# Performance work log

Hardware: AMD Instinct MI355X
Metric: run time of the kernel (lower is better)

The kernel has to match this reference:

```python
import jax, jax.numpy as jnp
import numpy as np

B, C, H, W = 4, 256, 160, 160
N = 512
REID = 128
NUM_LAYERS = 2
BINS = 7          # adaptive_avg_pool2d target (7,7)
EPS_BN = 1e-5
EPS_NORM = 1e-12  # torch F.normalize eps


def setup_inputs() -> dict:
    key = jax.random.key(0)
    ks = jax.random.split(key, 8)
    x = jax.random.normal(ks[0], (B, C, H, W), jnp.float32)
    # valid normalized boxes: x1,y1 in [0,0.7], w,h in [0.1,0.3]
    xy1 = jax.random.uniform(ks[1], (B, N, 2), minval=0.0, maxval=0.7)
    wh = jax.random.uniform(ks[2], (B, N, 2), minval=0.1, maxval=0.3)
    bboxes = jnp.concatenate([xy1, jnp.minimum(xy1 + wh, 1.0)], axis=-1)
    # conv stack params (kaiming-ish init), BN in eval mode with running stats
    conv_w = jax.random.normal(ks[3], (NUM_LAYERS, C, C, 3, 3), jnp.float32) * np.sqrt(2.0 / (C * 9)).astype(np.float32)
    conv_b = jnp.zeros((NUM_LAYERS, C), jnp.float32)
    bn_gamma = jnp.ones((NUM_LAYERS, C), jnp.float32)
    bn_beta = jnp.zeros((NUM_LAYERS, C), jnp.float32)
    bn_mean = jnp.zeros((NUM_LAYERS, C), jnp.float32)
    bn_var = jnp.ones((NUM_LAYERS, C), jnp.float32)
    # reid_embedding MLP: Linear(C, C//2) -> ReLU -> Dropout(eval) -> Linear(C//2, REID)
    w1 = jax.random.normal(ks[4], (C // 2, C), jnp.float32) * 0.01
    b1 = jnp.zeros((C // 2,), jnp.float32)
    w2 = jax.random.normal(ks[5], (REID, C // 2), jnp.float32) * 0.01
    b2 = jnp.zeros((REID,), jnp.float32)
    return dict(x=x, bboxes=bboxes, conv_w=conv_w, conv_b=conv_b,
                bn_gamma=bn_gamma, bn_beta=bn_beta, bn_mean=bn_mean, bn_var=bn_var,
                w1=w1, b1=b1, w2=w2, b2=b2)


def _conv_bn_relu(x, w, b, gamma, beta, mean, var):
    y = jax.lax.conv_general_dilated(
        x, w, window_strides=(1, 1), padding=((1, 1), (1, 1)),
        dimension_numbers=('NCHW', 'OIHW', 'NCHW')) + b[None, :, None, None]
    scale = (gamma / jnp.sqrt(var + EPS_BN))[None, :, None, None]
    y = (y - mean[None, :, None, None]) * scale + beta[None, :, None, None]
    return jax.nn.relu(y)


def _roi_pool(S, box):
    # S: (C, H+1, W+1) integral image of the feature map; box: (4,) = x1,y1,x2,y2 in [0,1]
    x1 = jnp.clip(jnp.floor(box[0] * W).astype(jnp.int32), 0, W)
    y1 = jnp.clip(jnp.floor(box[1] * H).astype(jnp.int32), 0, H)
    x2 = jnp.clip(jnp.floor(box[2] * W).astype(jnp.int32), 0, W)
    y2 = jnp.clip(jnp.floor(box[3] * H).astype(jnp.int32), 0, H)
    valid = (x2 > x1) & (y2 > y1)
    hl = jnp.maximum(y2 - y1, 1)
    wl = jnp.maximum(x2 - x1, 1)
    i = jnp.arange(BINS)
    # PyTorch adaptive_avg_pool2d binning: [floor(i*L/B), ceil((i+1)*L/B))
    hs = y1 + (i * hl) // BINS
    he = y1 + ((i + 1) * hl + BINS - 1) // BINS
    ws = x1 + (i * wl) // BINS
    we = x1 + ((i + 1) * wl + BINS - 1) // BINS
    # bin sums via integral image -> (C, 7, 7)
    s = (S[:, he[:, None], we[None, :]] - S[:, hs[:, None], we[None, :]]
         - S[:, he[:, None], ws[None, :]] + S[:, hs[:, None], ws[None, :]])
    area = ((he - hs)[:, None] * (we - ws)[None, :]).astype(S.dtype)
    # adaptive 7x7 avg pool, then global avg pool over the 7x7 grid
    pooled = jnp.mean(s / area, axis=(1, 2))  # (C,)
    return pooled, valid


def reference(x, bboxes, conv_w, conv_b, bn_gamma, bn_beta, bn_mean, bn_var, w1, b1, w2, b2):
    f = x
    for l in range(NUM_LAYERS):
        f = _conv_bn_relu(f, conv_w[l], conv_b[l], bn_gamma[l], bn_beta[l], bn_mean[l], bn_var[l])
    # integral image, zero-padded: S[b,c,y,x] = sum of f[b,c,:y,:x] -> (B, C, H+1, W+1)
    S = jnp.pad(jnp.cumsum(jnp.cumsum(f, axis=2), axis=3), ((0, 0), (0, 0), (1, 0), (1, 0)))
    pooled, valid = jax.vmap(jax.vmap(_roi_pool, in_axes=(None, 0)), in_axes=(0, 0))(S, bboxes)
    # reid_embedding MLP (dropout is identity in eval)
    h = jax.nn.relu(jnp.einsum('bnc,hc->bnh', pooled, w1) + b1)
    feat = jnp.einsum('bnh,rh->bnr', h, w2) + b2
    feat = jnp.where(valid[..., None], feat, jnp.zeros((), feat.dtype))
    norm = jnp.maximum(jnp.linalg.norm(feat, axis=-1, keepdims=True), EPS_NORM)
    return feat / norm
```

## Files before the change

### kernel.cpp

```cpp
#include <hip/hip_runtime.h>
#include <hip/hip_bf16.h>

typedef __attribute__((ext_vector_type(8))) short s16x8;
typedef __attribute__((ext_vector_type(4))) float f32x4;


__device__ __forceinline__ void async_ld16(const void* g, void* l) {
  __builtin_amdgcn_global_load_lds(
      (const __attribute__((address_space(1))) void*)g,
      (__attribute__((address_space(3))) void*)l, 16, 0, 0);
}

__global__ __launch_bounds__(256) void nchw2nhwc(const float* __restrict__ x,
                                                 __hip_bfloat16* __restrict__ xpad) {
  __shared__ float tile[32][33];
  int blk = blockIdx.x;
  int xt = blk % 5;
  int ct = (blk / 5) & 7;
  int by = blk / 40;
  int b = by / 160, y = by - (by / 160) * 160;
  int tx = threadIdx.x, ty = threadIdx.y;
  const float* src = x + (((size_t)(b * 256 + ct * 32)) * 160 + y) * 160 + xt * 32 + tx;
#pragma unroll
  for (int k = 0; k < 4; k++) tile[ty * 4 + k][tx] = src[(size_t)(ty * 4 + k) * 25600];
  __syncthreads();
  __hip_bfloat16* dst = xpad + (((size_t)(b * 162 + y + 1)) * 162 + (xt * 32 + 1)) * 256 + ct * 32 + tx;
#pragma unroll
  for (int k = 0; k < 4; k++) {
    int xx = ty * 4 + k;
    dst[(size_t)xx * 256] = __float2bfloat16(tile[tx][xx]);
  }
}

__global__ __launch_bounds__(256) void pack_w(const float* __restrict__ cw,
                                              __hip_bfloat16* __restrict__ wpk) {
  int t = blockIdx.x * 256 + threadIdx.x;
  int ci = t & 255, co = (t >> 8) & 255, rest = t >> 16;
  int tap = rest % 9, l = rest / 9;
  int dy = tap / 3, dx = tap - dy * 3;
  float v = cw[((((size_t)l * 256 + co) * 256 + ci) * 3 + dy) * 3 + dx];
  wpk[(((size_t)l * 9 + tap) * 256 + co) * 256 + ci] = __float2bfloat16(v);
}

__global__ void prep_bn(const float* __restrict__ cb, const float* __restrict__ g,
                        const float* __restrict__ bt, const float* __restrict__ mn,
                        const float* __restrict__ vr, float* __restrict__ ab) {
  int t = blockIdx.x * 256 + threadIdx.x;
  float a = g[t] / sqrtf(vr[t] + 1e-5f);
  ab[t] = a;
  ab[512 + t] = (cb[t] - mn[t]) * a + bt[t];
}

__global__ __launch_bounds__(256) void conv_bn_relu(
    const __hip_bfloat16* __restrict__ inp, __hip_bfloat16* __restrict__ outp,
    const __hip_bfloat16* __restrict__ wpk,
    const float* __restrict__ alpha, const float* __restrict__ beff) {
  __shared__ __align__(16) short As[128 * 64];
  __shared__ __align__(16) short Bs[128 * 64];
  const int t = threadIdx.x;
  const int logical = ((blockIdx.x & 7) * 200) + (blockIdx.x >> 3);
  const int mtile = logical >> 1;
  const int ntile = logical & 1;
  const int l = t & 63, wv = t >> 6;
  const int lr = l & 15, lq = l >> 4;
  const int wm = wv >> 1, wn = wv & 1;
  const int co0 = ntile << 7;

  const int srow = t >> 3;
  const int koff = (((t & 7) ^ (srow & 7)) << 3);
  const short* inS = (const short*)inp;
  const short* wS = (const short*)wpk;
  long abase[4];
#pragma unroll
  for (int i = 0; i < 4; i++) {
    int p = mtile * 128 + i * 32 + srow;
    int b = p / 25600; int r = p - b * 25600; int y = r / 160; int x = r - y * 160;
    abase[i] = (((long)b * 162 + y) * 162 + x) * 256 + koff;
  }
  const long bbase = ((long)(co0 + srow)) * 256 + koff;
  short* aldst = As + t * 8;
  short* bldst = Bs + t * 8;

  f32x4 acc[4][4];
#pragma unroll
  for (int i = 0; i < 4; i++)
#pragma unroll
    for (int j = 0; j < 4; j++) acc[i][j] = (f32x4){0.f, 0.f, 0.f, 0.f};

#pragma unroll 1
  for (int tap = 0; tap < 9; ++tap) {
    const int dy = tap / 3, dx = tap - dy * 3;
    const long atap = ((long)dy * 162 + dx) * 256;
    const long btap = (long)tap * 65536;
#pragma unroll
    for (int kc = 0; kc < 4; ++kc) {
      const long ko = (long)kc * 64;
      __syncthreads();
#pragma unroll
      for (int i = 0; i < 4; i++)
        async_ld16(inS + abase[i] + atap + ko, aldst + i * 2048);
#pragma unroll
      for (int i = 0; i < 4; i++)
        async_ld16(wS + bbase + btap + ko + i * 8192, bldst + i * 2048);
      __syncthreads();
#pragma unroll
      for (int kk = 0; kk < 2; ++kk) {
        const int ps = (((kk << 2) | lq) ^ (lr & 7)) << 3;
        s16x8 av[4], bv[4];
#pragma unroll
        for (int mi = 0; mi < 4; ++mi)
          av[mi] = *(const s16x8*)&As[(wm * 64 + mi * 16 + lr) * 64 + ps];
#pragma unroll
        for (int ni = 0; ni < 4; ++ni)
          bv[ni] = *(const s16x8*)&Bs[(wn * 64 + ni * 16 + lr) * 64 + ps];
#pragma unroll
        for (int mi = 0; mi < 4; ++mi)
#pragma unroll
          for (int ni = 0; ni < 4; ++ni)
            acc[mi][ni] = __builtin_amdgcn_mfma_f32_16x16x32_bf16(av[mi], bv[ni], acc[mi][ni], 0, 0, 0);
      }
    }
  }

  float al[4], be_[4];
#pragma unroll
  for (int ni = 0; ni < 4; ++ni) {
    int co = co0 + wn * 64 + ni * 16 + lr;
    al[ni] = alpha[co];
    be_[ni] = beff[co];
  }
#pragma unroll
  for (int mi = 0; mi < 4; ++mi) {
    int prow = mtile * 128 + wm * 64 + mi * 16 + lq * 4;
#pragma unroll
    for (int j = 0; j < 4; ++j) {
      int p = prow + j;
      int b = p / 25600; int r = p - b * 25600; int y = r / 160; int x = r - y * 160;
      long ob = (((long)b * 162 + (y + 1)) * 162 + (x + 1)) * 256 + co0 + wn * 64;
#pragma unroll
      for (int ni = 0; ni < 4; ++ni) {
        float v = acc[mi][ni][j] * al[ni] + be_[ni];
        outp[ob + ni * 16 + lr] = __float2bfloat16(fmaxf(v, 0.f));
      }
    }
  }
}

__global__ __launch_bounds__(256) void cumsum_w(const __hip_bfloat16* __restrict__ f2,
                                                float* __restrict__ S) {
  int bi = blockIdx.x;
  int b = bi / 160, y = bi - (bi / 160) * 160;
  int c = threadIdx.x;
  const __hip_bfloat16* src = f2 + (((size_t)b * 162 + (y + 1)) * 162 + 1) * 256 + c;
  float* dst = S + (((size_t)b * 161 + (y + 1)) * 161) * 256 + c;
  dst[0] = 0.f;
  float run = 0.f;
  for (int x4 = 0; x4 < 160; x4 += 4) {
    float v0 = __bfloat162float(src[(size_t)(x4 + 0) * 256]);
    float v1 = __bfloat162float(src[(size_t)(x4 + 1) * 256]);
    float v2 = __bfloat162float(src[(size_t)(x4 + 2) * 256]);
    float v3 = __bfloat162float(src[(size_t)(x4 + 3) * 256]);
    run += v0; dst[(size_t)(x4 + 1) * 256] = run;
    run += v1; dst[(size_t)(x4 + 2) * 256] = run;
    run += v2; dst[(size_t)(x4 + 3) * 256] = run;
    run += v3; dst[(size_t)(x4 + 4) * 256] = run;
  }
}

__global__ __launch_bounds__(256) void cumsum_h(float* __restrict__ S) {
  int bi = blockIdx.x;
  int b = bi / 161, q = bi - (bi / 161) * 161;
  int c = threadIdx.x;
  float* col = S + (((size_t)b * 161) * 161 + q) * 256 + c;
  const size_t ys = (size_t)161 * 256;
  col[0] = 0.f;
  float run = 0.f;
  for (int y0 = 1; y0 <= 160; y0 += 8) {
    float v[8];
#pragma unroll
    for (int k = 0; k < 8; k++) v[k] = col[(size_t)(y0 + k) * ys];
#pragma unroll
    for (int k = 0; k < 8; k++) { run += v[k]; col[(size_t)(y0 + k) * ys] = run; }
  }
}

__global__ __launch_bounds__(256) void roi_pool(const float* __restrict__ S,
                                                const float* __restrict__ bbox,
                                                float* __restrict__ pooled,
                                                int* __restrict__ valid) {
  int bn = blockIdx.x;
  int b = bn >> 9;
  int c = threadIdx.x;
  float bx1 = bbox[bn * 4 + 0], by1 = bbox[bn * 4 + 1];
  float bx2 = bbox[bn * 4 + 2], by2 = bbox[bn * 4 + 3];
  int x1 = min(max((int)floorf(bx1 * 160.f), 0), 160);
  int y1 = min(max((int)floorf(by1 * 160.f), 0), 160);
  int x2 = min(max((int)floorf(bx2 * 160.f), 0), 160);
  int y2 = min(max((int)floorf(by2 * 160.f), 0), 160);
  int vld = (x2 > x1 && y2 > y1) ? 1 : 0;
  int hl = max(y2 - y1, 1), wl = max(x2 - x1, 1);
  int hs[7], he[7], ws_[7], we_[7];
  float rh[7], rw[7];
#pragma unroll
  for (int i = 0; i < 7; i++) {
    hs[i] = y1 + (i * hl) / 7;
    he[i] = y1 + ((i + 1) * hl + 6) / 7;
    rh[i] = 1.f / (float)(he[i] - hs[i]);
    ws_[i] = x1 + (i * wl) / 7;
    we_[i] = x1 + ((i + 1) * wl + 6) / 7;
    rw[i] = 1.f / (float)(we_[i] - ws_[i]);
  }
  const float* Sb = S + (size_t)b * 161 * 161 * 256 + c;
  float acc = 0.f;
#pragma unroll
  for (int i = 0; i < 7; i++) {
    const float* rE = Sb + (size_t)he[i] * (161 * 256);
    const float* rS = Sb + (size_t)hs[i] * (161 * 256);
#pragma unroll
    for (int j = 0; j < 7; j++) {
      size_t qe = (size_t)we_[j] * 256, qs = (size_t)ws_[j] * 256;
      float s = rE[qe] - rS[qe] - rE[qs] + rS[qs];
      acc += s * (rh[i] * rw[j]);
    }
  }
  pooled[(size_t)bn * 256 + c] = acc * (1.f / 49.f);
  if (c == 0) valid[bn] = vld;
}

__global__ __launch_bounds__(128) void mlp_norm(const float* __restrict__ pooled,
                                                const int* __restrict__ valid,
                                                const float* __restrict__ w1,
                                                const float* __restrict__ b1,
                                                const float* __restrict__ w2,
                                                const float* __restrict__ b2,
                                                float* __restrict__ out) {
  int bn = blockIdx.x;
  int t = threadIdx.x;
  __shared__ float pl[256];
  __shared__ float hh[128];
  __shared__ float red[2];
  pl[t] = pooled[(size_t)bn * 256 + t];
  pl[t + 128] = pooled[(size_t)bn * 256 + 128 + t];
  __syncthreads();
  float a = b1[t];
  const float* w1r = w1 + (size_t)t * 256;
#pragma unroll 8
  for (int k = 0; k < 256; k++) a += w1r[k] * pl[k];
  hh[t] = fmaxf(a, 0.f);
  __syncthreads();
  float f = b2[t];
  const float* w2r = w2 + (size_t)t * 128;
#pragma unroll 8
  for (int k = 0; k < 128; k++) f += w2r[k] * hh[k];
  if (!valid[bn]) f = 0.f;
  float ss = f * f;
#pragma unroll
  for (int off = 32; off > 0; off >>= 1) ss += __shfl_xor(ss, off);
  if ((t & 63) == 0) red[t >> 6] = ss;
  __syncthreads();
  float nrm = fmaxf(sqrtf(red[0] + red[1]), 1e-12f);
  out[(size_t)bn * 128 + t] = f / nrm;
}

extern "C" void kernel_launch(void* const* d_in, const int* in_sizes, int n_in,
                              void* d_out, int out_size, void* d_ws, size_t ws_size,
                              hipStream_t stream) {
  const float* x = (const float*)d_in[0];
  const float* bboxes = (const float*)d_in[1];
  const float* conv_w = (const float*)d_in[2];
  const float* conv_b = (const float*)d_in[3];
  const float* bn_g = (const float*)d_in[4];
  const float* bn_b = (const float*)d_in[5];
  const float* bn_m = (const float*)d_in[6];
  const float* bn_v = (const float*)d_in[7];
  const float* w1 = (const float*)d_in[8];
  const float* b1 = (const float*)d_in[9];
  const float* w2 = (const float*)d_in[10];
  const float* b2 = (const float*)d_in[11];

  char* ws = (char*)d_ws;
  const size_t PADB = (size_t)4 * 162 * 162 * 256 * 2;
  const size_t WPKB = (size_t)2 * 9 * 256 * 256 * 2;
  const size_t SB = (size_t)4 * 161 * 161 * 256 * 4;

  __hip_bfloat16* xpad = (__hip_bfloat16*)(ws);
  __hip_bfloat16* f1 = (__hip_bfloat16*)(ws + PADB);
  __hip_bfloat16* wpk = (__hip_bfloat16*)(ws + 2 * PADB);
  float* abuf = (float*)(ws + 2 * PADB + WPKB);
  float* S = (float*)(ws + 2 * PADB + WPKB + 4096);
  float* pooled = (float*)(ws + 2 * PADB + WPKB + 4096 + SB);
  int* valid = (int*)(ws + 2 * PADB + WPKB + 4096 + SB + (size_t)4 * 512 * 256 * 4);

  hipMemsetAsync(ws, 0, 2 * PADB, stream);

  nchw2nhwc<<<25600, dim3(32, 8), 0, stream>>>(x, xpad);
  pack_w<<<4608, 256, 0, stream>>>(conv_w, wpk);
  prep_bn<<<2, 256, 0, stream>>>(conv_b, bn_g, bn_b, bn_m, bn_v, abuf);

  conv_bn_relu<<<1600, 256, 0, stream>>>(xpad, f1, wpk, abuf, abuf + 512);
  conv_bn_relu<<<1600, 256, 0, stream>>>(f1, xpad, wpk + (size_t)9 * 256 * 256, abuf + 256, abuf + 768);

  cumsum_w<<<640, 256, 0, stream>>>(xpad, S);
  cumsum_h<<<644, 256, 0, stream>>>(S);
  roi_pool<<<2048, 256, 0, stream>>>(S, bboxes, pooled, valid);
  mlp_norm<<<2048, 128, 0, stream>>>(pooled, valid, w1, b1, w2, b2, (float*)d_out);
}
```

Measured before the change: 485.7 us.

## Double-buffer conv LDS pipeline, zero only pad borders, vectorize cumsum, transpose MLP weights

The conv kernel now double-buffers its A/B LDS tiles and issues the next K-slice's async loads before computing the current one, with one barrier per step. It also raises MFMA priority and asks the compiler for two blocks per CU. The full memset of both padded buffers is replaced by a kernel that zeros only the one-pixel borders. cumsum_w reads bf16 pairs and writes float2, and the MLP weights are pre-transposed so per-thread loads coalesce. Together these target load latency in the dominant conv and bandwidth in the small kernels, at the cost of doubled LDS use per block (64 KB).

```diff
diff --git a/kernel.cpp b/kernel.cpp
--- a/kernel.cpp
+++ b/kernel.cpp
@@ -9,6 +9,20 @@
   __builtin_amdgcn_global_load_lds(
       (const __attribute__((address_space(1))) void*)g,
       (__attribute__((address_space(3))) void*)l, 16, 0, 0);
+}
+
+__global__ __launch_bounds__(256) void zero_borders(__hip_bfloat16* __restrict__ xpad,
+                                                    __hip_bfloat16* __restrict__ f1) {
+  int bi = blockIdx.x;
+  int buf = bi / 2576; int rem = bi - buf * 2576;
+  int b = rem / 644;   int e = rem - b * 644;
+  int y, x;
+  if (e < 162)      { y = 0;           x = e; }
+  else if (e < 324) { y = 161;         x = e - 162; }
+  else if (e < 484) { y = e - 324 + 1; x = 0; }
+  else              { y = e - 484 + 1; x = 161; }
+  __hip_bfloat16* p = (buf ? f1 : xpad) + (((size_t)b * 162 + y) * 162 + x) * 256 + threadIdx.x;
+  *p = __float2bfloat16(0.f);
 }
 
 __global__ __launch_bounds__(256) void nchw2nhwc(const float* __restrict__ x,
@@ -51,17 +65,33 @@
   ab[512 + t] = (cb[t] - mn[t]) * a + bt[t];
 }
 
-__global__ __launch_bounds__(256) void conv_bn_relu(
+__global__ __launch_bounds__(256) void pack_mlp(const float* __restrict__ w1,
+                                                const float* __restrict__ w2,
+                                                float* __restrict__ w1t,
+                                                float* __restrict__ w2t) {
+  int t = blockIdx.x * 256 + threadIdx.x;
+  if (t < 32768) {
+    int h = t >> 8, k = t & 255;
+    w1t[k * 128 + h] = w1[h * 256 + k];
+  } else {
+    int u = t - 32768;
+    int r = u >> 7, k = u & 127;
+    w2t[k * 128 + r] = w2[r * 128 + k];
+  }
+}
+
+__global__ __launch_bounds__(256, 2) void conv_bn_relu(
     const __hip_bfloat16* __restrict__ inp, __hip_bfloat16* __restrict__ outp,
     const __hip_bfloat16* __restrict__ wpk,
     const float* __restrict__ alpha, const float* __restrict__ beff) {
-  __shared__ __align__(16) short As[128 * 64];
-  __shared__ __align__(16) short Bs[128 * 64];
+  __shared__ __align__(16) short As[2 * 128 * 64];
+  __shared__ __align__(16) short Bs[2 * 128 * 64];
   const int t = threadIdx.x;
   const int logical = ((blockIdx.x & 7) * 200) + (blockIdx.x >> 3);
   const int mtile = logical >> 1;
   const int ntile = logical & 1;
-  const int l = t & 63, wv = t >> 6;
+  const int l = t & 63;
+  const int wv = t >> 6;
   const int lr = l & 15, lq = l >> 4;
   const int wm = wv >> 1, wn = wv & 1;
   const int co0 = ntile << 7;
@@ -78,8 +108,19 @@
     abase[i] = (((long)b * 162 + y) * 162 + x) * 256 + koff;
   }
   const long bbase = ((long)(co0 + srow)) * 256 + koff;
-  short* aldst = As + t * 8;
-  short* bldst = Bs + t * 8;
+
+  auto stage = [&](int u) {
+    const int tap = u >> 2;
+    const int dy = tap / 3, dx = tap - dy * 3;
+    const long atap = ((long)(dy * 162 + dx)) * 256 + (long)(u & 3) * 64;
+    const long btap = (long)tap * 65536 + (long)(u & 3) * 64;
+    short* ad = As + ((u & 1) << 13) + t * 8;
+    short* bd = Bs + ((u & 1) << 13) + t * 8;
+#pragma unroll
+    for (int i = 0; i < 4; i++) async_ld16(inS + abase[i] + atap, ad + i * 2048);
+#pragma unroll
+    for (int i = 0; i < 4; i++) async_ld16(wS + bbase + btap + i * 8192, bd + i * 2048);
+  };
 
   f32x4 acc[4][4];
 #pragma unroll
@@ -87,39 +128,33 @@
 #pragma unroll
     for (int j = 0; j < 4; j++) acc[i][j] = (f32x4){0.f, 0.f, 0.f, 0.f};
 
+  stage(0);
+  __syncthreads();
+
 #pragma unroll 1
-  for (int tap = 0; tap < 9; ++tap) {
-    const int dy = tap / 3, dx = tap - dy * 3;
-    const long atap = ((long)dy * 162 + dx) * 256;
-    const long btap = (long)tap * 65536;
-#pragma unroll
-    for (int kc = 0; kc < 4; ++kc) {
-      const long ko = (long)kc * 64;
-      __syncthreads();
-#pragma unroll
-      for (int i = 0; i < 4; i++)
-        async_ld16(inS + abase[i] + atap + ko, aldst + i * 2048);
-#pragma unroll
-      for (int i = 0; i < 4; i++)
-        async_ld16(wS + bbase + btap + ko + i * 8192, bldst + i * 2048);
-      __syncthreads();
-#pragma unroll
-      for (int kk = 0; kk < 2; ++kk) {
-        const int ps = (((kk << 2) | lq) ^ (lr & 7)) << 3;
-        s16x8 av[4], bv[4];
-#pragma unroll
-        for (int mi = 0; mi < 4; ++mi)
-          av[mi] = *(const s16x8*)&As[(wm * 64 + mi * 16 + lr) * 64 + ps];
+  for (int u = 0; u < 36; ++u) {
+    if (u < 35) stage(u + 1);
+    const short* Ab = As + ((u & 1) << 13);
+    const short* Bb = Bs + ((u & 1) << 13);
+#pragma unroll
+    for (int kk = 0; kk < 2; ++kk) {
+      const int ps = (((kk << 2) | lq) ^ (lr & 7)) << 3;
+      s16x8 av[4], bv[4];
+#pragma unroll
+      for (int mi = 0; mi < 4; ++mi)
+        av[mi] = *(const s16x8*)&Ab[(wm * 64 + mi * 16 + lr) * 64 + ps];
+#pragma unroll
+      for (int ni = 0; ni < 4; ++ni)
+        bv[ni] = *(const s16x8*)&Bb[(wn * 64 + ni * 16 + lr) * 64 + ps];
+      __builtin_amdgcn_s_setprio(1);
+#pragma unroll
+      for (int mi = 0; mi < 4; ++mi)
 #pragma unroll
         for (int ni = 0; ni < 4; ++ni)
-          bv[ni] = *(const s16x8*)&Bs[(wn * 64 + ni * 16 + lr) * 64 + ps];
-#pragma unroll
-        for (int mi = 0; mi < 4; ++mi)
-#pragma unroll
-          for (int ni = 0; ni < 4; ++ni)
-            acc[mi][ni] = __builtin_amdgcn_mfma_f32_16x16x32_bf16(av[mi], bv[ni], acc[mi][ni], 0, 0, 0);
-      }
+          acc[mi][ni] = __builtin_amdgcn_mfma_f32_16x16x32_bf16(av[mi], bv[ni], acc[mi][ni], 0, 0, 0);
+      __builtin_amdgcn_s_setprio(0);
     }
+    __syncthreads();
   }
 
   float al[4], be_[4];
@@ -148,22 +183,24 @@
 
 __global__ __launch_bounds__(256) void cumsum_w(const __hip_bfloat16* __restrict__ f2,
                                                 float* __restrict__ S) {
-  int bi = blockIdx.x;
-  int b = bi / 160, y = bi - (bi / 160) * 160;
-  int c = threadIdx.x;
-  const __hip_bfloat16* src = f2 + (((size_t)b * 162 + (y + 1)) * 162 + 1) * 256 + c;
-  float* dst = S + (((size_t)b * 161 + (y + 1)) * 161) * 256 + c;
-  dst[0] = 0.f;
-  float run = 0.f;
+  int row = blockIdx.x * 2 + (threadIdx.x >> 7);
+  int b = row / 160, y = row - (row / 160) * 160;
+  int cp = threadIdx.x & 127;
+  const unsigned* src =
+      (const unsigned*)((const short*)f2 + (((size_t)b * 162 + y + 1) * 162 + 1) * 256) + cp;
+  float2* dst = (float2*)(S + (((size_t)b * 161 + y + 1) * 161) * 256) + cp;
+  dst[0] = float2{0.f, 0.f};
+  float r0 = 0.f, r1 = 0.f;
   for (int x4 = 0; x4 < 160; x4 += 4) {
-    float v0 = __bfloat162float(src[(size_t)(x4 + 0) * 256]);
-    float v1 = __bfloat162float(src[(size_t)(x4 + 1) * 256]);
-    float v2 = __bfloat162float(src[(size_t)(x4 + 2) * 256]);
-    float v3 = __bfloat162float(src[(size_t)(x4 + 3) * 256]);
-    run += v0; dst[(size_t)(x4 + 1) * 256] = run;
-    run += v1; dst[(size_t)(x4 + 2) * 256] = run;
-    run += v2; dst[(size_t)(x4 + 3) * 256] = run;
-    run += v3; dst[(size_t)(x4 + 4) * 256] = run;
+    unsigned v[4];
+#pragma unroll
+    for (int k = 0; k < 4; k++) v[k] = src[(size_t)(x4 + k) * 128];
+#pragma unroll
+    for (int k = 0; k < 4; k++) {
+      r0 += __uint_as_float((v[k] & 0xffffu) << 16);
+      r1 += __uint_as_float(v[k] & 0xffff0000u);
+      dst[(size_t)(x4 + k + 1) * 128] = float2{r0, r1};
+    }
   }
 }
 
@@ -229,9 +266,9 @@
 
 __global__ __launch_bounds__(128) void mlp_norm(const float* __restrict__ pooled,
                                                 const int* __restrict__ valid,
-                                                const float* __restrict__ w1,
+                                                const float* __restrict__ w1t,
                                                 const float* __restrict__ b1,
-                                                const float* __restrict__ w2,
+                                                const float* __restrict__ w2t,
                                                 const float* __restrict__ b2,
                                                 float* __restrict__ out) {
   int bn = blockIdx.x;
@@ -243,15 +280,13 @@
   pl[t + 128] = pooled[(size_t)bn * 256 + 128 + t];
   __syncthreads();
   float a = b1[t];
-  const float* w1r = w1 + (size_t)t * 256;
 #pragma unroll 8
-  for (int k = 0; k < 256; k++) a += w1r[k] * pl[k];
+  for (int k = 0; k < 256; k++) a += w1t[k * 128 + t] * pl[k];
   hh[t] = fmaxf(a, 0.f);
   __syncthreads();
   float f = b2[t];
-  const float* w2r = w2 + (size_t)t * 128;
 #pragma unroll 8
-  for (int k = 0; k < 128; k++) f += w2r[k] * hh[k];
+  for (int k = 0; k < 128; k++) f += w2t[k * 128 + t] * hh[k];
   if (!valid[bn]) f = 0.f;
   float ss = f * f;
 #pragma unroll
@@ -282,6 +317,7 @@
   const size_t PADB = (size_t)4 * 162 * 162 * 256 * 2;
   const size_t WPKB = (size_t)2 * 9 * 256 * 256 * 2;
   const size_t SB = (size_t)4 * 161 * 161 * 256 * 4;
+  const size_t PLB = (size_t)4 * 512 * 256 * 4;
 
   __hip_bfloat16* xpad = (__hip_bfloat16*)(ws);
   __hip_bfloat16* f1 = (__hip_bfloat16*)(ws + PADB);
@@ -289,19 +325,21 @@
   float* abuf = (float*)(ws + 2 * PADB + WPKB);
   float* S = (float*)(ws + 2 * PADB + WPKB + 4096);
   float* pooled = (float*)(ws + 2 * PADB + WPKB + 4096 + SB);
-  int* valid = (int*)(ws + 2 * PADB + WPKB + 4096 + SB + (size_t)4 * 512 * 256 * 4);
-
-  hipMemsetAsync(ws, 0, 2 * PADB, stream);
-
+  int* valid = (int*)(ws + 2 * PADB + WPKB + 4096 + SB + PLB);
+  float* w1t = (float*)(ws + 2 * PADB + WPKB + 4096 + SB + PLB + 8192);
+  float* w2t = w1t + 32768;
+
+  zero_borders<<<5152, 256, 0, stream>>>(xpad, f1);
   nchw2nhwc<<<25600, dim3(32, 8), 0, stream>>>(x, xpad);
   pack_w<<<4608, 256, 0, stream>>>(conv_w, wpk);
   prep_bn<<<2, 256, 0, stream>>>(conv_b, bn_g, bn_b, bn_m, bn_v, abuf);
+  pack_mlp<<<192, 256, 0, stream>>>(w1, w2, w1t, w2t);
 
   conv_bn_relu<<<1600, 256, 0, stream>>>(xpad, f1, wpk, abuf, abuf + 512);
   conv_bn_relu<<<1600, 256, 0, stream>>>(f1, xpad, wpk + (size_t)9 * 256 * 256, abuf + 256, abuf + 768);
 
-  cumsum_w<<<640, 256, 0, stream>>>(xpad, S);
+  cumsum_w<<<320, 256, 0, stream>>>(xpad, S);
   cumsum_h<<<644, 256, 0, stream>>>(S);
   roi_pool<<<2048, 256, 0, stream>>>(S, bboxes, pooled, valid);
-  mlp_norm<<<2048, 128, 0, stream>>>(pooled, valid, w1, b1, w2, b2, (float*)d_out);
-}
+  mlp_norm<<<2048, 128, 0, stream>>>(pooled, valid, w1t, b1, w2t, b2, (float*)d_out);
+}
```

Measured after the change: 459.7 us. 5.3% less time.
